# Kernel optimization log

Measured on AMD Instinct MI355X. Metric: run time of the kernel, lower is better.

Reference implementation:

```python
import jax, jax.numpy as jnp
import numpy as np

POOL_SIZES = (1, 3, 6, 8)
EPS = 1e-5


def conv1x1(x, W, b):
    # x: [b, cin, h, w], W: [cout, cin], b: [cout]
    return jnp.einsum('bchw,oc->bohw', x, W) + b[None, :, None, None]


def ppm(x):
    # x: [b, c, h, w] -> [b, c, S] with S = sum(p*p); H,W divisible by each p
    b, c, h, w = x.shape
    outs = []
    for p in POOL_SIZES:
        pooled = x.reshape(b, c, p, h // p, p, w // p).mean(axis=(3, 5))
        outs.append(pooled.reshape(b, c, p * p))
    return jnp.concatenate(outs, axis=-1)


def setup_inputs() -> dict:
    key = jax.random.key(0)
    ks = jax.random.split(key, 8)
    B, Cin, H, W = 4, 512, 120, 120
    Ck, Cv, Cout = 256, 256, 512
    x = jax.random.normal(ks[0], (B, Cin, H, W), dtype=jnp.float32)
    sc = lambda cin: 1.0 / np.sqrt(cin)
    Wk = jax.random.normal(ks[1], (Ck, Cin), dtype=jnp.float32) * sc(Cin)
    bk = jnp.zeros((Ck,), jnp.float32)
    gamma = jnp.ones((Ck,), jnp.float32)
    beta = jnp.zeros((Ck,), jnp.float32)
    mean = jax.random.normal(ks[2], (Ck,), dtype=jnp.float32) * 0.1
    var = jax.random.uniform(ks[3], (Ck,), dtype=jnp.float32, minval=0.5, maxval=1.5)
    Wv = jax.random.normal(ks[4], (Cv, Cin), dtype=jnp.float32) * sc(Cin)
    bv = jnp.zeros((Cv,), jnp.float32)
    # original inits Conv_Out to zero; use random weights for a nontrivial baseline
    Wo = jax.random.normal(ks[5], (Cout, Cv), dtype=jnp.float32) * sc(Cv)
    bo = jnp.zeros((Cout,), jnp.float32)
    return {'x': x, 'Wk': Wk, 'bk': bk, 'gamma': gamma, 'beta': beta,
            'mean': mean, 'var': var, 'Wv': Wv, 'bv': bv, 'Wo': Wo, 'bo': bo}


def reference(x, Wk, bk, gamma, beta, mean, var, Wv, bv, Wo, bo):
    b, _, h, w = x.shape
    ck = Wk.shape[0]
    cv = Wv.shape[0]
    # shared Conv_Key / Conv_Query: conv1x1 -> BN (inference) -> ReLU
    kq = conv1x1(x, Wk, bk)
    inv = gamma / jnp.sqrt(var + EPS)
    kq = jax.nn.relu(kq * inv[None, :, None, None] + (beta - mean * inv)[None, :, None, None])
    value = ppm(conv1x1(x, Wv, bv)).transpose(0, 2, 1)      # [b, S, cv]
    key = ppm(kq)                                            # [b, ck, S]
    query = kq.reshape(b, ck, h * w).transpose(0, 2, 1)      # [b, hw, ck]
    scores = jnp.einsum('bnc,bcs->bns', query, key) * (ck ** -0.5)
    attn = jax.nn.softmax(scores, axis=-1)                   # [b, hw, S]
    agg = jnp.einsum('bns,bsv->bnv', attn, value)            # [b, hw, cv]
    agg = agg.transpose(0, 2, 1).reshape(b, cv, h, w)
    return conv1x1(agg, Wo, bo)
```

## Files before the change

### kernel.cpp

```cpp
#include <hip/hip_runtime.h>
#include <cstdint>
#include <cstddef>

#define HW 14400
#define WIDTH 120
#define S_TOT 110

typedef unsigned short u16;
typedef __attribute__((ext_vector_type(8))) short bf16x8;
typedef __attribute__((ext_vector_type(4))) float f32x4;

__device__ __forceinline__ u16 f2bf(float x) {
  unsigned u = __float_as_uint(x);
  unsigned r = (u + 0x7fffu + ((u >> 16) & 1u)) >> 16;
  return (u16)r;
}
__device__ __forceinline__ float bf2f(u16 h) {
  return __uint_as_float((unsigned)h << 16);
}

__device__ __forceinline__ void async16(void* lds, const void* g) {
  __builtin_amdgcn_global_load_lds(
      (const __attribute__((address_space(1))) void*)g,
      (__attribute__((address_space(3))) void*)lds, 16, 0, 0);
}

__device__ __forceinline__ float pool_scale(int s) {
  return (s == 0) ? (1.f / 14400.f)
         : (s < 10) ? (1.f / 1600.f)
         : (s < 46) ? (1.f / 400.f)
                    : (1.f / 225.f);
}

__global__ __launch_bounds__(256) void pool_kernel(const float* __restrict__ in,
                                                   float* __restrict__ outp) {
  __shared__ float colsum[2880];
  __shared__ float part[576];
  const float* plane = in + (size_t)blockIdx.x * HW;
  int t = threadIdx.x;
  for (int i = t; i < 2880; i += 256) {
    int by = i / 120, x = i - by * 120;
    const float* p0 = plane + (by * 5) * WIDTH + x;
    colsum[i] = p0[0] + p0[WIDTH] + p0[2 * WIDTH] + p0[3 * WIDTH] + p0[4 * WIDTH];
  }
  __syncthreads();
  for (int bb = t; bb < 576; bb += 256) {
    int by = bb / 24, bx = bb - by * 24;
    const float* c = &colsum[by * 120 + bx * 5];
    part[bb] = c[0] + c[1] + c[2] + c[3] + c[4];
  }
  __syncthreads();
  if (t < S_TOT) {
    float s = 0.f;
    if (t == 0) {
      for (int i = 0; i < 576; ++i) s += part[i];
      s *= (1.f / 14400.f);
    } else if (t < 10) {
      int idx = t - 1, i = idx / 3, j = idx % 3;
      for (int a = 0; a < 8; ++a)
        for (int c = 0; c < 8; ++c) s += part[(i * 8 + a) * 24 + (j * 8 + c)];
      s *= (1.f / 1600.f);
    } else if (t < 46) {
      int idx = t - 10, i = idx / 6, j = idx % 6;
      for (int a = 0; a < 4; ++a)
        for (int c = 0; c < 4; ++c) s += part[(i * 4 + a) * 24 + (j * 4 + c)];
      s *= (1.f / 400.f);
    } else {
      int idx = t - 46, i = idx / 8, j = idx % 8;
      for (int a = 0; a < 3; ++a)
        for (int c = 0; c < 3; ++c) s += part[(i * 3 + a) * 24 + (j * 3 + c)];
      s *= (1.f / 225.f);
    }
    outp[(size_t)blockIdx.x * S_TOT + t] = s;
  }
}

__global__ __launch_bounds__(256) void convert_w(const float* __restrict__ in,
                                                 u16* __restrict__ hi,
                                                 u16* __restrict__ lo, int n) {
  int i = blockIdx.x * 256 + threadIdx.x;
  if (i < n) {
    float v = in[i];
    u16 h = f2bf(v);
    hi[i] = h;
    lo[i] = f2bf(v - bf2f(h));
  }
}

template <int CIN>
__global__ __launch_bounds__(256) void convert_t(const float* __restrict__ X,
                                                 u16* __restrict__ xth,
                                                 u16* __restrict__ xtl) {
  __shared__ float ls[64][65];
  int b = blockIdx.z;
  int n0 = blockIdx.x * 64, k0 = blockIdx.y * 64;
  int t = threadIdx.x;
  int rt = t >> 4, c4 = (t & 15) * 4;
#pragma unroll
  for (int rr = 0; rr < 4; ++rr) {
    int kk = rr * 16 + rt;
    float4 v = *(const float4*)&X[((size_t)(b * CIN + k0 + kk)) * HW + n0 + c4];
    ls[kk][c4] = v.x; ls[kk][c4 + 1] = v.y; ls[kk][c4 + 2] = v.z; ls[kk][c4 + 3] = v.w;
  }
  __syncthreads();
#pragma unroll
  for (int rr = 0; rr < 4; ++rr) {
    int nn = rr * 16 + rt;
    float v0 = ls[c4 + 0][nn], v1 = ls[c4 + 1][nn], v2 = ls[c4 + 2][nn], v3 = ls[c4 + 3][nn];
    ushort4 oh, ol;
    oh.x = f2bf(v0); ol.x = f2bf(v0 - bf2f(oh.x));
    oh.y = f2bf(v1); ol.y = f2bf(v1 - bf2f(oh.y));
    oh.z = f2bf(v2); ol.z = f2bf(v2 - bf2f(oh.z));
    oh.w = f2bf(v3); ol.w = f2bf(v3 - bf2f(oh.w));
    size_t idx = ((size_t)(b * HW + n0 + nn)) * CIN + k0 + c4;
    *(ushort4*)&xth[idx] = oh;
    *(ushort4*)&xtl[idx] = ol;
  }
}

template <int K, int M_TOT, bool BNRELU>
__global__ __launch_bounds__(512, 2) void gemm_mfma(
    const u16* __restrict__ Ah, const u16* __restrict__ Al,
    const u16* __restrict__ Bh, const u16* __restrict__ Bl,
    float* __restrict__ C,
    const float* __restrict__ p0, const float* __restrict__ p1,
    const float* __restrict__ p2, const float* __restrict__ p3,
    const float* __restrict__ p4,
    u16* __restrict__ Th, u16* __restrict__ Tl) {
  constexpr int NSTEP = K / 32;
  __shared__ alignas(16) u16 smem[61440];

  int t = threadIdx.x, w = t >> 6, l = t & 63;
  int wm = w >> 2, wn = w & 3;
  int b = blockIdx.z;
  int n0 = blockIdx.x * 192;
  int m0 = blockIdx.y * 128;

  int fr = l & 15, fkc = l >> 4;
  const size_t bOff = (size_t)b * HW;

  auto stage = [&](int ks, int slot) {
    int k0 = ks * 32;
#pragma unroll
    for (int c = 0; c < 5; ++c) {
      int i = w * 5 + c;
      const u16* g;
      u16* d;
      if (i < 8) {
        g = Ah + (size_t)(m0 + i * 16 + fr) * K + k0 + fkc * 8;
        d = &smem[slot * 8192 + i * 512];
      } else if (i < 16) {
        g = Al + (size_t)(m0 + (i - 8) * 16 + fr) * K + k0 + fkc * 8;
        d = &smem[slot * 8192 + i * 512];
      } else if (i < 28) {
        g = Bh + (bOff + n0 + (i - 16) * 16 + fr) * (size_t)K + k0 + fkc * 8;
        d = &smem[24576 + slot * 12288 + (i - 16) * 512];
      } else {
        g = Bl + (bOff + n0 + (i - 28) * 16 + fr) * (size_t)K + k0 + fkc * 8;
        d = &smem[24576 + slot * 12288 + (i - 16) * 512];
      }
      async16(d, g);
    }
  };

  f32x4 acc[4][3];
#pragma unroll
  for (int i = 0; i < 4; ++i)
#pragma unroll
    for (int j = 0; j < 3; ++j) acc[i][j] = (f32x4){0.f, 0.f, 0.f, 0.f};

  stage(0, 0);
  stage(1, 1);

  for (int ks = 0; ks < NSTEP; ++ks) {
    if (ks + 1 < NSTEP)
      asm volatile("s_waitcnt vmcnt(5)" ::: "memory");
    else
      asm volatile("s_waitcnt vmcnt(0)" ::: "memory");
    __builtin_amdgcn_s_barrier();
    __builtin_amdgcn_sched_barrier(0);

    if (ks + 2 < NSTEP) stage(ks + 2, (ks + 2) % 3);

    int cur = ks % 3;
    bf16x8 bh[3], bl[3];
#pragma unroll
    for (int nt = 0; nt < 3; ++nt) {
      bh[nt] = *(const bf16x8*)&smem[24576 + cur * 12288 + (wn * 3 + nt) * 512 + l * 8];
      bl[nt] = *(const bf16x8*)&smem[24576 + cur * 12288 + (12 + wn * 3 + nt) * 512 + l * 8];
    }
    bf16x8 ah[4], al[4];
#pragma unroll
    for (int mt = 0; mt < 4; ++mt) {
      ah[mt] = *(const bf16x8*)&smem[cur * 8192 + (wm * 4 + mt) * 512 + l * 8];
      al[mt] = *(const bf16x8*)&smem[cur * 8192 + (8 + wm * 4 + mt) * 512 + l * 8];
    }
    __builtin_amdgcn_s_setprio(1);
#pragma unroll
    for (int mt = 0; mt < 4; ++mt)
#pragma unroll
      for (int nt = 0; nt < 3; ++nt) {
        acc[mt][nt] = __builtin_amdgcn_mfma_f32_16x16x32_bf16(ah[mt], bh[nt], acc[mt][nt], 0, 0, 0);
        acc[mt][nt] = __builtin_amdgcn_mfma_f32_16x16x32_bf16(ah[mt], bl[nt], acc[mt][nt], 0, 0, 0);
        acc[mt][nt] = __builtin_amdgcn_mfma_f32_16x16x32_bf16(al[mt], bh[nt], acc[mt][nt], 0, 0, 0);
      }
    __builtin_amdgcn_s_setprio(0);
  }

  __syncthreads();

  int q4 = (l >> 4) * 4;
#pragma unroll
  for (int mt = 0; mt < 4; ++mt) {
    int mb = m0 + (wm * 4 + mt) * 16 + q4;
    float iv[4], ad[4];
    if (BNRELU) {
      float4 g0 = *(const float4*)&p0[mb];
      float4 g1 = *(const float4*)&p1[mb];
      float4 g2 = *(const float4*)&p2[mb];
      float4 g3 = *(const float4*)&p3[mb];
      float4 g4 = *(const float4*)&p4[mb];
      iv[0] = g1.x * rsqrtf(g4.x + 1e-5f);
      iv[1] = g1.y * rsqrtf(g4.y + 1e-5f);
      iv[2] = g1.z * rsqrtf(g4.z + 1e-5f);
      iv[3] = g1.w * rsqrtf(g4.w + 1e-5f);
      ad[0] = (g0.x - g3.x) * iv[0] + g2.x;
      ad[1] = (g0.y - g3.y) * iv[1] + g2.y;
      ad[2] = (g0.z - g3.z) * iv[2] + g2.z;
      ad[3] = (g0.w - g3.w) * iv[3] + g2.w;
    } else {
      float4 g0 = *(const float4*)&p0[mb];
      ad[0] = g0.x; ad[1] = g0.y; ad[2] = g0.z; ad[3] = g0.w;
    }
#pragma unroll
    for (int nt = 0; nt < 3; ++nt) {
      int n = n0 + (wn * 3 + nt) * 16 + fr;
      float v[4];
#pragma unroll
      for (int r = 0; r < 4; ++r) {
        float x = acc[mt][nt][r];
        v[r] = BNRELU ? fmaxf(x * iv[r] + ad[r], 0.f) : x + ad[r];
        if (C) C[((size_t)(b * M_TOT) + mb + r) * HW + n] = v[r];
      }
      if (BNRELU && Th) {
        ushort4 hh, ll;
        hh.x = f2bf(v[0]); ll.x = f2bf(v[0] - bf2f(hh.x));
        hh.y = f2bf(v[1]); ll.y = f2bf(v[1] - bf2f(hh.y));
        hh.z = f2bf(v[2]); ll.z = f2bf(v[2] - bf2f(hh.z));
        hh.w = f2bf(v[3]); ll.w = f2bf(v[3] - bf2f(hh.w));
        int nl = (wn * 3 + nt) * 16 + fr;
        int ml = (wm * 4 + mt) * 16 + q4;
        *(ushort4*)&smem[nl * 136 + ml] = hh;
        *(ushort4*)&smem[26112 + nl * 136 + ml] = ll;
      }
    }
  }
  if (BNRELU && Th) {
    __syncthreads();
#pragma unroll
    for (int it = 0; it < 6; ++it) {
      int row = it * 32 + (t >> 4);
      int c8 = (t & 15) * 8;
      size_t go = (bOff + n0 + row) * (size_t)M_TOT + m0 + c8;
      *(bf16x8*)&Th[go] = *(const bf16x8*)&smem[row * 136 + c8];
      *(bf16x8*)&Tl[go] = *(const bf16x8*)&smem[26112 + row * 136 + c8];
    }
  }
}

__global__ __launch_bounds__(512) void gemm_kq_fx(
    const u16* __restrict__ Ah, const u16* __restrict__ Al,
    const float* __restrict__ X,
    float* __restrict__ C,
    const float* __restrict__ p0, const float* __restrict__ p1,
    const float* __restrict__ p2, const float* __restrict__ p3,
    const float* __restrict__ p4,
    u16* __restrict__ Th, u16* __restrict__ Tl) {
  constexpr int NSTEP = 16;
  __shared__ alignas(16) u16 smem[52224];

  int t = threadIdx.x, w = t >> 6, l = t & 63;
  int wm = w >> 2, wn = w & 3;
  int b = blockIdx.z;
  int n0 = blockIdx.x * 192;
  int m0 = blockIdx.y * 128;
  int fr = l & 15, fkc = l >> 4;
  const size_t bOff = (size_t)b * HW;
  const float* xb = X + (size_t)b * 512 * HW + n0;

  int kc4v[3], nnv[3], wOffH[3];
#pragma unroll
  for (int j = 0; j < 3; ++j) {
    int s = t + j * 512;
    kc4v[j] = s / 192;
    nnv[j] = s - kc4v[j] * 192;
    wOffH[j] = (nnv[j] >> 4) * 512 + (((kc4v[j] >> 1) * 16 + (nnv[j] & 15)) * 8) +
               (kc4v[j] & 1) * 4;
  }

  auto stageA = [&](int ks, int slot) {
    int k0 = ks * 32;
#pragma unroll
    for (int c = 0; c < 2; ++c) {
      int i = w * 2 + c;
      const u16* g = (i < 8)
          ? Ah + (size_t)(m0 + i * 16 + fr) * 512 + k0 + fkc * 8
          : Al + (size_t)(m0 + (i - 8) * 16 + fr) * 512 + k0 + fkc * 8;
      async16(&smem[slot * 8192 + i * 512], g);
    }
  };

  auto issueB = [&](int ks, float* r) {
#pragma unroll
    for (int j = 0; j < 3; ++j) {
      const float* src = xb + (size_t)(ks * 32 + kc4v[j] * 4) * HW + nnv[j];
#pragma unroll
      for (int i = 0; i < 4; ++i) r[j * 4 + i] = src[(size_t)i * HW];
    }
  };

  auto cvtB = [&](float* r, int buf) {
#pragma unroll
    for (int j = 0; j < 3; ++j) {
      ushort4 hh, ll;
      float v0 = r[j * 4 + 0], v1 = r[j * 4 + 1], v2 = r[j * 4 + 2], v3 = r[j * 4 + 3];
      hh.x = f2bf(v0); ll.x = f2bf(v0 - bf2f(hh.x));
      hh.y = f2bf(v1); ll.y = f2bf(v1 - bf2f(hh.y));
      hh.z = f2bf(v2); ll.z = f2bf(v2 - bf2f(hh.z));
      hh.w = f2bf(v3); ll.w = f2bf(v3 - bf2f(hh.w));
      int o = 24576 + buf * 12288 + wOffH[j];
      *(ushort4*)&smem[o] = hh;
      *(ushort4*)&smem[o + 12 * 512] = ll;
    }
  };

  f32x4 acc[4][3];
#pragma unroll
  for (int i = 0; i < 4; ++i)
#pragma unroll
    for (int j = 0; j < 3; ++j) acc[i][j] = (f32x4){0.f, 0.f, 0.f, 0.f};

  float rB0[12], rB1[12];
  stageA(0, 0); issueB(0, rB0);
  stageA(1, 1); issueB(1, rB1);
  __builtin_amdgcn_sched_barrier(0);
  asm volatile("s_waitcnt vmcnt(14)" ::: "memory");
  cvtB(rB0, 0);

#pragma unroll 2
  for (int ks = 0; ks < NSTEP; ++ks) {
    asm volatile("s_waitcnt lgkmcnt(0)" ::: "memory");
    __builtin_amdgcn_s_barrier();
    __builtin_amdgcn_sched_barrier(0);

    if (ks + 2 < NSTEP) {
      stageA(ks + 2, (ks + 2) % 3);
      issueB(ks + 2, (ks & 1) ? rB1 : rB0);
      __builtin_amdgcn_sched_barrier(0);
    }

    int curA = ks % 3, curB = ks & 1;
    bf16x8 bh[3], bl[3];
#pragma unroll
    for (int nt = 0; nt < 3; ++nt) {
      bh[nt] = *(const bf16x8*)&smem[24576 + curB * 12288 + (wn * 3 + nt) * 512 + l * 8];
      bl[nt] = *(const bf16x8*)&smem[24576 + curB * 12288 + (12 + wn * 3 + nt) * 512 + l * 8];
    }
    bf16x8 ah[4], al[4];
#pragma unroll
    for (int mt = 0; mt < 4; ++mt) {
      ah[mt] = *(const bf16x8*)&smem[curA * 8192 + (wm * 4 + mt) * 512 + l * 8];
      al[mt] = *(const bf16x8*)&smem[curA * 8192 + (8 + wm * 4 + mt) * 512 + l * 8];
    }
    __builtin_amdgcn_s_setprio(1);
#pragma unroll
    for (int mt = 0; mt < 4; ++mt)
#pragma unroll
      for (int nt = 0; nt < 3; ++nt) {
        acc[mt][nt] = __builtin_amdgcn_mfma_f32_16x16x32_bf16(ah[mt], bh[nt], acc[mt][nt], 0, 0, 0);
        acc[mt][nt] = __builtin_amdgcn_mfma_f32_16x16x32_bf16(ah[mt], bl[nt], acc[mt][nt], 0, 0, 0);
        acc[mt][nt] = __builtin_amdgcn_mfma_f32_16x16x32_bf16(al[mt], bh[nt], acc[mt][nt], 0, 0, 0);
      }
    __builtin_amdgcn_s_setprio(0);

    if (ks + 1 < NSTEP) {
      if (ks + 2 < NSTEP)
        asm volatile("s_waitcnt vmcnt(14)" ::: "memory");
      else
        asm volatile("s_waitcnt vmcnt(0)" ::: "memory");
      cvtB((ks & 1) ? rB0 : rB1, (ks + 1) & 1);
    }
  }

  __syncthreads();

  int q4 = (l >> 4) * 4;
#pragma unroll
  for (int mt = 0; mt < 4; ++mt) {
    int mb = m0 + (wm * 4 + mt) * 16 + q4;
    float iv[4], ad[4];
    {
      float4 g0 = *(const float4*)&p0[mb];
      float4 g1 = *(const float4*)&p1[mb];
      float4 g2 = *(const float4*)&p2[mb];
      float4 g3 = *(const float4*)&p3[mb];
      float4 g4 = *(const float4*)&p4[mb];
      iv[0] = g1.x * rsqrtf(g4.x + 1e-5f);
      iv[1] = g1.y * rsqrtf(g4.y + 1e-5f);
      iv[2] = g1.z * rsqrtf(g4.z + 1e-5f);
      iv[3] = g1.w * rsqrtf(g4.w + 1e-5f);
      ad[0] = (g0.x - g3.x) * iv[0] + g2.x;
      ad[1] = (g0.y - g3.y) * iv[1] + g2.y;
      ad[2] = (g0.z - g3.z) * iv[2] + g2.z;
      ad[3] = (g0.w - g3.w) * iv[3] + g2.w;
    }
#pragma unroll
    for (int nt = 0; nt < 3; ++nt) {
      int n = n0 + (wn * 3 + nt) * 16 + fr;
      float v[4];
#pragma unroll
      for (int r = 0; r < 4; ++r) {
        float x = acc[mt][nt][r];
        v[r] = fmaxf(x * iv[r] + ad[r], 0.f);
        if (C) C[((size_t)(b * 256) + mb + r) * HW + n] = v[r];
      }
      ushort4 hh, ll;
      hh.x = f2bf(v[0]); ll.x = f2bf(v[0] - bf2f(hh.x));
      hh.y = f2bf(v[1]); ll.y = f2bf(v[1] - bf2f(hh.y));
      hh.z = f2bf(v[2]); ll.z = f2bf(v[2] - bf2f(hh.z));
      hh.w = f2bf(v[3]); ll.w = f2bf(v[3] - bf2f(hh.w));
      int nl = (wn * 3 + nt) * 16 + fr;
      int ml = (wm * 4 + mt) * 16 + q4;
      *(ushort4*)&smem[nl * 136 + ml] = hh;
      *(ushort4*)&smem[26112 + nl * 136 + ml] = ll;
    }
  }
  __syncthreads();
#pragma unroll
  for (int it = 0; it < 6; ++it) {
    int row = it * 32 + (t >> 4);
    int c8 = (t & 15) * 8;
    size_t go = (bOff + n0 + row) * (size_t)256 + m0 + c8;
    *(bf16x8*)&Th[go] = *(const bf16x8*)&smem[row * 136 + c8];
    *(bf16x8*)&Tl[go] = *(const bf16x8*)&smem[26112 + row * 136 + c8];
  }
}

__global__ __launch_bounds__(256) void pool_kqt(const u16* __restrict__ kqth,
                                                const u16* __restrict__ kqtl,
                                                float* __restrict__ keypsum) {
  int cq = blockIdx.x, band = blockIdx.y, b = blockIdx.z;
  int t = threadIdx.x;
  int row0 = band * 5, col0 = cq * 30;
  int r3 = row0 / 40, r6 = row0 / 20, r8 = row0 / 15;
  float* base = keypsum + (size_t)b * 110 * 256 + t;
  float s1 = 0.f, s3 = 0.f, s6 = 0.f, s8 = 0.f;
  int b3 = -1, b6 = -1, b8 = -1;
  for (int cc = 0; cc < 30; ++cc) {
    int col = col0 + cc;
    float v = 0.f;
#pragma unroll
    for (int r = 0; r < 5; ++r) {
      size_t o = ((size_t)(b * HW + (row0 + r) * 120 + col)) * 256 + t;
      v += bf2f(kqth[o]) + bf2f(kqtl[o]);
    }
    int i3 = 1 + r3 * 3 + col / 40;
    int i6 = 10 + r6 * 6 + col / 20;
    int i8 = 46 + r8 * 8 + col / 15;
    s1 += v;
    if (i3 != b3) { if (b3 >= 0) atomicAdd(base + (size_t)b3 * 256, s3); s3 = 0.f; b3 = i3; }
    s3 += v;
    if (i6 != b6) { if (b6 >= 0) atomicAdd(base + (size_t)b6 * 256, s6); s6 = 0.f; b6 = i6; }
    s6 += v;
    if (i8 != b8) { if (b8 >= 0) atomicAdd(base + (size_t)b8 * 256, s8); s8 = 0.f; b8 = i8; }
    s8 += v;
  }
  atomicAdd(base, s1);
  atomicAdd(base + (size_t)b3 * 256, s3);
  atomicAdd(base + (size_t)b6 * 256, s6);
  atomicAdd(base + (size_t)b8 * 256, s8);
}

__global__ __launch_bounds__(256) void value_kernel(
    const float* __restrict__ Wv, const float* __restrict__ xp,
    const float* __restrict__ bv, u16* __restrict__ vth,
    u16* __restrict__ vtl) {
  int b = blockIdx.x >> 7, s = blockIdx.x & 127;
  int t = threadIdx.x;
  size_t o = ((size_t)(b * 256 + t)) * 128 + s;
  if (s >= S_TOT) { vth[o] = 0; vtl[o] = 0; return; }
  __shared__ float xs[512];
  for (int i = t; i < 512; i += 256) xs[i] = xp[((size_t)b * 512 + i) * S_TOT + s];
  __syncthreads();
  float accv = 0.f;
  const float* wv = Wv + (size_t)t * 512;
  for (int k = 0; k < 512; k += 4) {
    float4 w4 = *(const float4*)&wv[k];
    accv += w4.x * xs[k] + w4.y * xs[k + 1] + w4.z * xs[k + 2] + w4.w * xs[k + 3];
  }
  accv += bv[t];
  u16 h = f2bf(accv);
  vth[o] = h;
  vtl[o] = f2bf(accv - bf2f(h));
}

template <int SUMLAYOUT>
__global__ __launch_bounds__(256) void convert_key(const float* __restrict__ keyp,
                                                   u16* __restrict__ kth,
                                                   u16* __restrict__ ktl) {
  int b = blockIdx.x;
  int t = threadIdx.x;
  for (int i = t; i < 128 * 256; i += 256) {
    int s = i >> 8, c = i & 255;
    float v = 0.f;
    if (s < S_TOT) {
      if (SUMLAYOUT)
        v = keyp[((size_t)(b * 110 + s)) * 256 + c] * pool_scale(s);
      else
        v = keyp[((size_t)(b * 256 + c)) * S_TOT + s];
    }
    u16 h = f2bf(v);
    size_t o = ((size_t)(b * 128 + s)) * 256 + c;
    kth[o] = h;
    ktl[o] = f2bf(v - bf2f(h));
  }
}

__global__ __launch_bounds__(256) void attn_mfma(
    const u16* __restrict__ qh, const u16* __restrict__ ql,
    const u16* __restrict__ kh, const u16* __restrict__ kl,
    const u16* __restrict__ vh, const u16* __restrict__ vl,
    u16* __restrict__ aggh, u16* __restrict__ aggl) {
  __shared__ alignas(16) u16 lds[17408];
  int b = blockIdx.y, pix0 = blockIdx.x * 64;
  int t = threadIdx.x, w = t >> 6, l = t & 63;
  int fr = l & 15, q = l >> 4;

  const u16* kbase_h = kh + (size_t)b * 128 * 256;
  const u16* kbase_l = kl + (size_t)b * 128 * 256;

  f32x4 acc[8];
#pragma unroll
  for (int st = 0; st < 8; ++st) acc[st] = (f32x4){0.f, 0.f, 0.f, 0.f};

  const u16* qbh = qh + ((size_t)(b * HW + pix0 + w * 16 + fr)) * 256 + q * 8;
  const u16* qbl = ql + ((size_t)(b * HW + pix0 + w * 16 + fr)) * 256 + q * 8;

  auto stageK = [&](int ks, int buf) {
    int c0 = ks * 32;
#pragma unroll
    for (int j = 0; j < 4; ++j) {
      int i = t + j * 256;
      int half = i >> 9;
      int idx = i & 511;
      int st = idx >> 6, ll = idx & 63;
      const u16* src = (half ? kbase_l : kbase_h) +
                       (st * 16 + (ll & 15)) * 256 + c0 + (ll >> 4) * 8;
      async16(&lds[buf * 8192 + half * 4096 + idx * 8], src);
    }
  };

  stageK(0, 0);
  for (int ks = 0; ks < 8; ++ks) {
    __syncthreads();
    if (ks < 7) stageK(ks + 1, (ks + 1) & 1);
    bf16x8 ah = *(const bf16x8*)(qbh + ks * 32);
    bf16x8 al = *(const bf16x8*)(qbl + ks * 32);
    const u16* kb = &lds[(ks & 1) * 8192 + l * 8];
#pragma unroll
    for (int st = 0; st < 8; ++st) {
      bf16x8 bh = *(const bf16x8*)(kb + st * 512);
      bf16x8 bl = *(const bf16x8*)(kb + 4096 + st * 512);
      acc[st] = __builtin_amdgcn_mfma_f32_16x16x32_bf16(ah, bh, acc[st], 0, 0, 0);
      acc[st] = __builtin_amdgcn_mfma_f32_16x16x32_bf16(ah, bl, acc[st], 0, 0, 0);
      acc[st] = __builtin_amdgcn_mfma_f32_16x16x32_bf16(al, bh, acc[st], 0, 0, 0);
    }
  }

#pragma unroll
  for (int st = 0; st < 8; ++st)
#pragma unroll
    for (int r = 0; r < 4; ++r) acc[st][r] *= 0.0625f;
  if (fr >= 14) {
#pragma unroll
    for (int r = 0; r < 4; ++r) acc[6][r] = -1e30f;
  }
#pragma unroll
  for (int r = 0; r < 4; ++r) acc[7][r] = -1e30f;

#pragma unroll
  for (int r = 0; r < 4; ++r) {
    float m = -1e30f;
#pragma unroll
    for (int st = 0; st < 8; ++st) m = fmaxf(m, acc[st][r]);
    m = fmaxf(m, __shfl_xor(m, 1));
    m = fmaxf(m, __shfl_xor(m, 2));
    m = fmaxf(m, __shfl_xor(m, 4));
    m = fmaxf(m, __shfl_xor(m, 8));
    float s = 0.f;
#pragma unroll
    for (int st = 0; st < 8; ++st) {
      float e = __expf(acc[st][r] - m);
      acc[st][r] = e;
      s += e;
    }
    s += __shfl_xor(s, 1);
    s += __shfl_xor(s, 2);
    s += __shfl_xor(s, 4);
    s += __shfl_xor(s, 8);
    float inv = 1.f / s;
#pragma unroll
    for (int st = 0; st < 8; ++st) acc[st][r] *= inv;
  }

  __syncthreads();

  int prow = w * 16 + q * 4;
#pragma unroll
  for (int st = 0; st < 8; ++st) {
    int s = st * 16 + fr;
#pragma unroll
    for (int r = 0; r < 4; ++r) {
      float v = acc[st][r];
      u16 h = f2bf(v);
      lds[(prow + r) * 136 + s] = h;
      lds[8704 + (prow + r) * 136 + s] = f2bf(v - bf2f(h));
    }
  }
  __syncthreads();

  f32x4 oacc[4][4];
#pragma unroll
  for (int nt = 0; nt < 4; ++nt)
#pragma unroll
    for (int pt = 0; pt < 4; ++pt) oacc[nt][pt] = (f32x4){0.f, 0.f, 0.f, 0.f};

  const u16* vbh = vh + ((size_t)(b * 256 + w * 64 + fr)) * 128 + q * 8;
  const u16* vbl = vl + ((size_t)(b * 256 + w * 64 + fr)) * 128 + q * 8;

#pragma unroll
  for (int kc = 0; kc < 4; ++kc) {
    bf16x8 ph[4], pl[4];
#pragma unroll
    for (int pt = 0; pt < 4; ++pt) {
      ph[pt] = *(const bf16x8*)&lds[(pt * 16 + fr) * 136 + kc * 32 + q * 8];
      pl[pt] = *(const bf16x8*)&lds[8704 + (pt * 16 + fr) * 136 + kc * 32 + q * 8];
    }
#pragma unroll
    for (int nt = 0; nt < 4; ++nt) {
      bf16x8 a_h = *(const bf16x8*)(vbh + (size_t)nt * 16 * 128 + kc * 32);
      bf16x8 a_l = *(const bf16x8*)(vbl + (size_t)nt * 16 * 128 + kc * 32);
#pragma unroll
      for (int pt = 0; pt < 4; ++pt) {
        oacc[nt][pt] = __builtin_amdgcn_mfma_f32_16x16x32_bf16(a_h, ph[pt], oacc[nt][pt], 0, 0, 0);
        oacc[nt][pt] = __builtin_amdgcn_mfma_f32_16x16x32_bf16(a_h, pl[pt], oacc[nt][pt], 0, 0, 0);
        oacc[nt][pt] = __builtin_amdgcn_mfma_f32_16x16x32_bf16(a_l, ph[pt], oacc[nt][pt], 0, 0, 0);
      }
    }
  }

#pragma unroll
  for (int nt = 0; nt < 4; ++nt) {
#pragma unroll
    for (int pt = 0; pt < 4; ++pt) {
      ushort4 oh, ol;
      float v0 = oacc[nt][pt][0], v1 = oacc[nt][pt][1];
      float v2 = oacc[nt][pt][2], v3 = oacc[nt][pt][3];
      oh.x = f2bf(v0); ol.x = f2bf(v0 - bf2f(oh.x));
      oh.y = f2bf(v1); ol.y = f2bf(v1 - bf2f(oh.y));
      oh.z = f2bf(v2); ol.z = f2bf(v2 - bf2f(oh.z));
      oh.w = f2bf(v3); ol.w = f2bf(v3 - bf2f(oh.w));
      size_t o = ((size_t)(b * HW + pix0 + pt * 16 + fr)) * 256 + (w * 4 + nt) * 16 + q * 4;
      *(ushort4*)&aggh[o] = oh;
      *(ushort4*)&aggl[o] = ol;
    }
  }
}

extern "C" void kernel_launch(void* const* d_in, const int* in_sizes, int n_in,
                              void* d_out, int out_size, void* d_ws, size_t ws_size,
                              hipStream_t stream) {
  (void)in_sizes; (void)n_in; (void)out_size;
  const float* x     = (const float*)d_in[0];
  const float* Wk    = (const float*)d_in[1];
  const float* bk    = (const float*)d_in[2];
  const float* gamma = (const float*)d_in[3];
  const float* beta  = (const float*)d_in[4];
  const float* mean  = (const float*)d_in[5];
  const float* var   = (const float*)d_in[6];
  const float* Wv    = (const float*)d_in[7];
  const float* bv    = (const float*)d_in[8];
  const float* Wo    = (const float*)d_in[9];
  const float* bo    = (const float*)d_in[10];
  float* out = (float*)d_out;

  char* p = (char*)d_ws;
  float* kq = (float*)p;      p += (size_t)14745600 * 4;
  u16* xth = (u16*)p;         p += (size_t)29491200 * 2;
  u16* xtl = (u16*)p;         p += (size_t)29491200 * 2;
  u16* wkh = (u16*)p;         p += 131072 * 2;
  u16* wkl = (u16*)p;         p += 131072 * 2;
  u16* woh = (u16*)p;         p += 131072 * 2;
  u16* wol = (u16*)p;         p += 131072 * 2;
  float* xp = (float*)p;      p += (size_t)4 * 512 * 110 * 4;
  float* keypsum = (float*)p; p += (size_t)4 * 110 * 256 * 4;
  u16* vth = (u16*)p;         p += (size_t)4 * 256 * 128 * 2;
  u16* vtl = (u16*)p;         p += (size_t)4 * 256 * 128 * 2;
  u16* kth = (u16*)p;         p += (size_t)4 * 128 * 256 * 2;
  u16* ktl = (u16*)p;         p += (size_t)4 * 128 * 256 * 2;
  u16* kqth_f = (u16*)p;      p += (size_t)14745600 * 2;
  u16* kqtl_f = (u16*)p;      p += (size_t)14745600 * 2;
  bool fused = ((size_t)(p - (char*)d_ws) <= ws_size);

  u16* aggh = xth;
  u16* aggl = xtl;
  u16* kqth = fused ? kqth_f : xth + (size_t)14745600;
  u16* kqtl = fused ? kqtl_f : xtl + (size_t)14745600;

  if (fused)
    hipMemsetAsync(keypsum, 0, (size_t)4 * 110 * 256 * 4, stream);

  convert_w<<<512, 256, 0, stream>>>(Wk, wkh, wkl, 256 * 512);
  convert_w<<<512, 256, 0, stream>>>(Wo, woh, wol, 512 * 256);
  pool_kernel<<<dim3(4 * 512), dim3(256), 0, stream>>>(x, xp);
  value_kernel<<<dim3(4 * 128), 256, 0, stream>>>(Wv, xp, bv, vth, vtl);
  if (fused) {
    gemm_kq_fx<<<dim3(75, 2, 4), 512, 0, stream>>>(
        wkh, wkl, x, nullptr, bk, gamma, beta, mean, var, kqth, kqtl);
    pool_kqt<<<dim3(4, 24, 4), 256, 0, stream>>>(kqth, kqtl, keypsum);
    convert_key<1><<<dim3(4), dim3(256), 0, stream>>>(keypsum, kth, ktl);
  } else {
    convert_t<512><<<dim3(225, 8, 4), 256, 0, stream>>>(x, xth, xtl);
    gemm_mfma<512, 256, true><<<dim3(75, 2, 4), 512, 0, stream>>>(
        wkh, wkl, xth, xtl, kq, bk, gamma, beta, mean, var, kqth, kqtl);
    convert_t<256><<<dim3(225, 4, 4), 256, 0, stream>>>(kq, kqth, kqtl);
    pool_kernel<<<dim3(4 * 256), dim3(256), 0, stream>>>(kq, keypsum);
    convert_key<0><<<dim3(4), dim3(256), 0, stream>>>(keypsum, kth, ktl);
  }
  attn_mfma<<<dim3(225, 4), 256, 0, stream>>>(kqth, kqtl, kth, ktl, vth, vtl,
                                              aggh, aggl);
  gemm_mfma<256, 512, false><<<dim3(75, 4, 4), 512, 0, stream>>>(
      woh, wol, aggh, aggl, out, bo, nullptr, nullptr, nullptr, nullptr,
      nullptr, nullptr);
}
```

Baseline: 524.2 us.

## Fuse attention and output 1x1 conv into a single MFMA kernel

Adds attn_out_mfma, which computes scores, softmax and the value aggregation, then stages the aggregated tile in LDS and applies the Wo projection plus bias directly, writing the final output. This removes the round trip of the split-bf16 aggregated activations through global memory and one kernel launch on the fused path. In exchange the Wo weights are re-read per 64-pixel block from global/L2, register pressure rises (oacc 16 accumulators plus acc2), and the output stores are strided per pixel row, which may coalesce poorly.

```diff
diff --git a/kernel.cpp b/kernel.cpp
--- a/kernel.cpp
+++ b/kernel.cpp
@@ -526,6 +526,209 @@
   }
 }
 
+__global__ __launch_bounds__(256) void attn_out_mfma(
+    const u16* __restrict__ qh, const u16* __restrict__ ql,
+    const u16* __restrict__ kh, const u16* __restrict__ kl,
+    const u16* __restrict__ vh, const u16* __restrict__ vl,
+    const u16* __restrict__ woh, const u16* __restrict__ wol,
+    const float* __restrict__ bo, float* __restrict__ out) {
+  __shared__ alignas(16) u16 lds[17408];
+  int b = blockIdx.y, pix0 = blockIdx.x * 64;
+  int t = threadIdx.x, w = t >> 6, l = t & 63;
+  int fr = l & 15, q = l >> 4;
+
+  const u16* kbase_h = kh + (size_t)b * 128 * 256;
+  const u16* kbase_l = kl + (size_t)b * 128 * 256;
+
+  f32x4 acc[8];
+#pragma unroll
+  for (int st = 0; st < 8; ++st) acc[st] = (f32x4){0.f, 0.f, 0.f, 0.f};
+
+  const u16* qbh = qh + ((size_t)(b * HW + pix0 + w * 16 + fr)) * 256 + q * 8;
+  const u16* qbl = ql + ((size_t)(b * HW + pix0 + w * 16 + fr)) * 256 + q * 8;
+
+  auto stageK = [&](int ks, int buf) {
+    int c0 = ks * 32;
+#pragma unroll
+    for (int j = 0; j < 4; ++j) {
+      int i = t + j * 256;
+      int half = i >> 9;
+      int idx = i & 511;
+      int st = idx >> 6, ll = idx & 63;
+      const u16* src = (half ? kbase_l : kbase_h) +
+                       (st * 16 + (ll & 15)) * 256 + c0 + (ll >> 4) * 8;
+      async16(&lds[buf * 8192 + half * 4096 + idx * 8], src);
+    }
+  };
+
+  stageK(0, 0);
+  for (int ks = 0; ks < 8; ++ks) {
+    __syncthreads();
+    if (ks < 7) stageK(ks + 1, (ks + 1) & 1);
+    bf16x8 ah = *(const bf16x8*)(qbh + ks * 32);
+    bf16x8 al = *(const bf16x8*)(qbl + ks * 32);
+    const u16* kb = &lds[(ks & 1) * 8192 + l * 8];
+#pragma unroll
+    for (int st = 0; st < 8; ++st) {
+      bf16x8 bh = *(const bf16x8*)(kb + st * 512);
+      bf16x8 bl = *(const bf16x8*)(kb + 4096 + st * 512);
+      acc[st] = __builtin_amdgcn_mfma_f32_16x16x32_bf16(ah, bh, acc[st], 0, 0, 0);
+      acc[st] = __builtin_amdgcn_mfma_f32_16x16x32_bf16(ah, bl, acc[st], 0, 0, 0);
+      acc[st] = __builtin_amdgcn_mfma_f32_16x16x32_bf16(al, bh, acc[st], 0, 0, 0);
+    }
+  }
+
+#pragma unroll
+  for (int st = 0; st < 8; ++st)
+#pragma unroll
+    for (int r = 0; r < 4; ++r) acc[st][r] *= 0.0625f;
+  if (fr >= 14) {
+#pragma unroll
+    for (int r = 0; r < 4; ++r) acc[6][r] = -1e30f;
+  }
+#pragma unroll
+  for (int r = 0; r < 4; ++r) acc[7][r] = -1e30f;
+
+#pragma unroll
+  for (int r = 0; r < 4; ++r) {
+    float m = -1e30f;
+#pragma unroll
+    for (int st = 0; st < 8; ++st) m = fmaxf(m, acc[st][r]);
+    m = fmaxf(m, __shfl_xor(m, 1));
+    m = fmaxf(m, __shfl_xor(m, 2));
+    m = fmaxf(m, __shfl_xor(m, 4));
+    m = fmaxf(m, __shfl_xor(m, 8));
+    float s = 0.f;
+#pragma unroll
+    for (int st = 0; st < 8; ++st) {
+      float e = __expf(acc[st][r] - m);
+      acc[st][r] = e;
+      s += e;
+    }
+    s += __shfl_xor(s, 1);
+    s += __shfl_xor(s, 2);
+    s += __shfl_xor(s, 4);
+    s += __shfl_xor(s, 8);
+    float inv = 1.f / s;
+#pragma unroll
+    for (int st = 0; st < 8; ++st) acc[st][r] *= inv;
+  }
+
+  __syncthreads();
+
+  int prow = w * 16 + q * 4;
+#pragma unroll
+  for (int st = 0; st < 8; ++st) {
+    int s = st * 16 + fr;
+#pragma unroll
+    for (int r = 0; r < 4; ++r) {
+      float v = acc[st][r];
+      u16 h = f2bf(v);
+      lds[(prow + r) * 136 + s] = h;
+      lds[8704 + (prow + r) * 136 + s] = f2bf(v - bf2f(h));
+    }
+  }
+  __syncthreads();
+
+  f32x4 oacc[4][4];
+#pragma unroll
+  for (int nt = 0; nt < 4; ++nt)
+#pragma unroll
+    for (int pt = 0; pt < 4; ++pt) oacc[nt][pt] = (f32x4){0.f, 0.f, 0.f, 0.f};
+
+  const u16* vbh = vh + ((size_t)(b * 256 + w * 64 + fr)) * 128 + q * 8;
+  const u16* vbl = vl + ((size_t)(b * 256 + w * 64 + fr)) * 128 + q * 8;
+
+#pragma unroll
+  for (int kc = 0; kc < 4; ++kc) {
+    bf16x8 ph[4], pl[4];
+#pragma unroll
+    for (int pt = 0; pt < 4; ++pt) {
+      ph[pt] = *(const bf16x8*)&lds[(pt * 16 + fr) * 136 + kc * 32 + q * 8];
+      pl[pt] = *(const bf16x8*)&lds[8704 + (pt * 16 + fr) * 136 + kc * 32 + q * 8];
+    }
+#pragma unroll
+    for (int nt = 0; nt < 4; ++nt) {
+      bf16x8 a_h = *(const bf16x8*)(vbh + (size_t)nt * 16 * 128 + kc * 32);
+      bf16x8 a_l = *(const bf16x8*)(vbl + (size_t)nt * 16 * 128 + kc * 32);
+#pragma unroll
+      for (int pt = 0; pt < 4; ++pt) {
+        oacc[nt][pt] = __builtin_amdgcn_mfma_f32_16x16x32_bf16(a_h, ph[pt], oacc[nt][pt], 0, 0, 0);
+        oacc[nt][pt] = __builtin_amdgcn_mfma_f32_16x16x32_bf16(a_h, pl[pt], oacc[nt][pt], 0, 0, 0);
+        oacc[nt][pt] = __builtin_amdgcn_mfma_f32_16x16x32_bf16(a_l, ph[pt], oacc[nt][pt], 0, 0, 0);
+      }
+    }
+  }
+
+  const u16* wbh = woh + ((size_t)(w * 128 + fr)) * 256 + q * 8;
+  const u16* wbl = wol + ((size_t)(w * 128 + fr)) * 256 + q * 8;
+#pragma unroll
+  for (int h = 0; h < 2; ++h) {
+    __syncthreads();
+#pragma unroll
+    for (int pt2 = 0; pt2 < 2; ++pt2) {
+      int row = pt2 * 16 + fr;
+#pragma unroll
+      for (int nt = 0; nt < 4; ++nt) {
+        float v0 = oacc[nt][h * 2 + pt2][0], v1 = oacc[nt][h * 2 + pt2][1];
+        float v2 = oacc[nt][h * 2 + pt2][2], v3 = oacc[nt][h * 2 + pt2][3];
+        ushort4 hh, ll;
+        hh.x = f2bf(v0); ll.x = f2bf(v0 - bf2f(hh.x));
+        hh.y = f2bf(v1); ll.y = f2bf(v1 - bf2f(hh.y));
+        hh.z = f2bf(v2); ll.z = f2bf(v2 - bf2f(hh.z));
+        hh.w = f2bf(v3); ll.w = f2bf(v3 - bf2f(hh.w));
+        int col = (w * 4 + nt) * 16 + q * 4;
+        *(ushort4*)&lds[row * 264 + col] = hh;
+        *(ushort4*)&lds[8448 + row * 264 + col] = ll;
+      }
+    }
+    __syncthreads();
+#pragma unroll
+    for (int g2 = 0; g2 < 2; ++g2) {
+      f32x4 acc2[4][2];
+#pragma unroll
+      for (int i = 0; i < 4; ++i) {
+        acc2[i][0] = (f32x4){0.f, 0.f, 0.f, 0.f};
+        acc2[i][1] = (f32x4){0.f, 0.f, 0.f, 0.f};
+      }
+#pragma unroll
+      for (int kc = 0; kc < 8; ++kc) {
+        bf16x8 bh2[2], bl2[2];
+#pragma unroll
+        for (int pt2 = 0; pt2 < 2; ++pt2) {
+          bh2[pt2] = *(const bf16x8*)&lds[(pt2 * 16 + fr) * 264 + kc * 32 + q * 8];
+          bl2[pt2] = *(const bf16x8*)&lds[8448 + (pt2 * 16 + fr) * 264 + kc * 32 + q * 8];
+        }
+#pragma unroll
+        for (int n4 = 0; n4 < 4; ++n4) {
+          int nt2 = g2 * 4 + n4;
+          bf16x8 a_h = *(const bf16x8*)(wbh + (size_t)nt2 * 16 * 256 + kc * 32);
+          bf16x8 a_l = *(const bf16x8*)(wbl + (size_t)nt2 * 16 * 256 + kc * 32);
+#pragma unroll
+          for (int pt2 = 0; pt2 < 2; ++pt2) {
+            acc2[n4][pt2] = __builtin_amdgcn_mfma_f32_16x16x32_bf16(a_h, bh2[pt2], acc2[n4][pt2], 0, 0, 0);
+            acc2[n4][pt2] = __builtin_amdgcn_mfma_f32_16x16x32_bf16(a_h, bl2[pt2], acc2[n4][pt2], 0, 0, 0);
+            acc2[n4][pt2] = __builtin_amdgcn_mfma_f32_16x16x32_bf16(a_l, bh2[pt2], acc2[n4][pt2], 0, 0, 0);
+          }
+        }
+      }
+#pragma unroll
+      for (int n4 = 0; n4 < 4; ++n4) {
+        int ob = w * 128 + (g2 * 4 + n4) * 16 + q * 4;
+        float4 g = *(const float4*)&bo[ob];
+#pragma unroll
+        for (int pt2 = 0; pt2 < 2; ++pt2) {
+          int pix = pix0 + (h * 2 + pt2) * 16 + fr;
+          out[((size_t)(b * 512) + ob + 0) * HW + pix] = acc2[n4][pt2][0] + g.x;
+          out[((size_t)(b * 512) + ob + 1) * HW + pix] = acc2[n4][pt2][1] + g.y;
+          out[((size_t)(b * 512) + ob + 2) * HW + pix] = acc2[n4][pt2][2] + g.z;
+          out[((size_t)(b * 512) + ob + 3) * HW + pix] = acc2[n4][pt2][3] + g.w;
+        }
+      }
+    }
+  }
+}
+
 __global__ __launch_bounds__(256) void attn_mfma(
     const u16* __restrict__ qh, const u16* __restrict__ ql,
     const u16* __restrict__ kh, const u16* __restrict__ kl,
@@ -729,6 +932,8 @@
         wkh, wkl, x, nullptr, bk, gamma, beta, mean, var, kqth, kqtl);
     pool_kqt<<<dim3(4, 24, 4), 256, 0, stream>>>(kqth, kqtl, keypsum);
     convert_key<1><<<dim3(4), dim3(256), 0, stream>>>(keypsum, kth, ktl);
+    attn_out_mfma<<<dim3(225, 4), 256, 0, stream>>>(
+        kqth, kqtl, kth, ktl, vth, vtl, woh, wol, bo, out);
   } else {
     convert_t<512><<<dim3(225, 8, 4), 256, 0, stream>>>(x, xth, xtl);
     gemm_mfma<512, 256, true><<<dim3(75, 2, 4), 512, 0, stream>>>(
@@ -736,10 +941,10 @@
     convert_t<256><<<dim3(225, 4, 4), 256, 0, stream>>>(kq, kqth, kqtl);
     pool_kernel<<<dim3(4 * 256), dim3(256), 0, stream>>>(kq, keypsum);
     convert_key<0><<<dim3(4), dim3(256), 0, stream>>>(keypsum, kth, ktl);
-  }
-  attn_mfma<<<dim3(225, 4), 256, 0, stream>>>(kqth, kqtl, kth, ktl, vth, vtl,
-                                              aggh, aggl);
-  gemm_mfma<256, 512, false><<<dim3(75, 4, 4), 512, 0, stream>>>(
-      woh, wol, aggh, aggl, out, bo, nullptr, nullptr, nullptr, nullptr,
-      nullptr, nullptr);
-}
+    attn_mfma<<<dim3(225, 4), 256, 0, stream>>>(kqth, kqtl, kth, ktl, vth, vtl,
+                                                aggh, aggl);
+    gemm_mfma<256, 512, false><<<dim3(75, 4, 4), 512, 0, stream>>>(
+        woh, wol, aggh, aggl, out, bo, nullptr, nullptr, nullptr, nullptr,
+        nullptr, nullptr);
+  }
+}
```

Result: slower. 600.1 us (+14.5%).
